# Kernel optimization log

Measured on AMD Instinct MI355X. Metric: run time of the kernel, lower is better.

The kernel has to match this reference:

```python
import jax, jax.numpy as jnp
import numpy as np

B, S, L = 256, 512, 128


def setup_inputs() -> dict:
    key = jax.random.key(0)
    k0, k1, k2, k3, k4, k5 = jax.random.split(key, 6)
    features = jax.random.normal(k0, (B, S, L), dtype=jnp.float32)
    attention_mask = jnp.ones((B, S), dtype=jnp.int32)  # all positions valid
    labels = jax.random.randint(k1, (B, S), 0, L)
    confidence = jax.random.uniform(k2, (B,), dtype=jnp.float32)
    start_transitions = jax.random.uniform(k3, (L,), minval=-0.1, maxval=0.1)
    end_transitions = jax.random.uniform(k4, (L,), minval=-0.1, maxval=0.1)
    transitions = jax.random.uniform(k5, (L, L), minval=-0.1, maxval=0.1)
    return {
        "features": features,
        "start_transitions": start_transitions,
        "end_transitions": end_transitions,
        "transitions": transitions,
        "confidence": confidence,
        "attention_mask": attention_mask,
        "labels": labels,
    }


def _crf_loss(features, start_transitions, end_transitions, transitions,
              confidence, attention_mask, labels):
    # time-major, matching torch.swapaxes(features, 0, 1)
    feats = jnp.swapaxes(features, 0, 1)                    # [S,B,L]
    mask = jnp.swapaxes(attention_mask, 0, 1).astype(bool)  # [S,B]
    labs = jnp.swapaxes(jnp.where(labels == -100, 0, labels), 0, 1)  # [S,B]
    bs = feats.shape[1]
    barange = jnp.arange(bs)

    # ---- log numerator (gold path score), fully vectorized over time ----
    emit = jnp.take_along_axis(feats, labs[:, :, None], axis=2)[..., 0]  # [S,B]
    trans_scores = transitions[labs[:-1], labs[1:]]                      # [S-1,B]
    maskf = mask[1:].astype(feats.dtype)
    log_num = (start_transitions[labs[0]] + emit[0]
               + jnp.sum((trans_scores + emit[1:]) * maskf, axis=0))
    seq_lens = mask.sum(axis=0) - 1                                      # [B]
    last_tags = labs[seq_lens, barange]
    log_num = log_num + end_transitions[last_tags]

    # ---- log denominator (partition function) via sequential scan ----
    def step(alpha, xs):
        feat_t, mask_t = xs  # [B,L], [B]
        nxt = jax.nn.logsumexp(
            alpha[:, :, None] + transitions[None, :, :] + feat_t[:, None, :],
            axis=1)
        return jnp.where(mask_t[:, None], nxt, alpha), None

    alpha0 = start_transitions + feats[0]                    # [B,L]
    alpha, _ = jax.lax.scan(step, alpha0, (feats[1:], mask[1:]))
    log_den = jax.nn.logsumexp(alpha + end_transitions, axis=1)  # [B]

    loss = (log_den - log_num) * confidence
    return jnp.mean(loss)


def reference(features, start_transitions, end_transitions, transitions,
              confidence, attention_mask, labels):
    return _crf_loss(features, start_transitions, end_transitions, transitions,
                     confidence, attention_mask, labels)
```

## Files before the change

kernel.cpp:

```cpp
#include <hip/hip_runtime.h>
#include <hip/hip_bf16.h>
#include <math.h>

#define NB 256
#define SS 512
#define LL 128

typedef short bf16x8 __attribute__((ext_vector_type(8)));
typedef float f32x4 __attribute__((ext_vector_type(4)));

__device__ __forceinline__ short f2bf(float f) {
    __hip_bfloat16 h = __float2bfloat16(f);
    short s;
    __builtin_memcpy(&s, &h, 2);
    return s;
}

#define MFMA1632(c, a, bb) \
    c = __builtin_amdgcn_mfma_f32_16x16x32_bf16(a, bb, c, 0, 0, 0)

template <int ISB>
__device__ __forceinline__ void run_chain(
    const int lane,
    const float* __restrict__ fb,
    const float* __restrict__ start_t,
    const float* __restrict__ end_t,
    const float* __restrict__ trans,
    float* __restrict__ eRing,
    const int* __restrict__ lmask,
    float* __restrict__ outv,
    float* __restrict__ oute)
{
    const int lo = lane & 15;
    const int hi = lane >> 4;

    bf16x8 Af[8][4];
#pragma unroll
    for (int nt = 0; nt < 8; ++nt) {
#pragma unroll
        for (int kt = 0; kt < 4; ++kt) {
            bf16x8 fr;
#pragma unroll
            for (int j = 0; j < 8; ++j) {
                const int r = 32 * kt + 16 * (j >> 2) + 4 * hi + (j & 3);
                const int n = 16 * nt + lo;
                const float tv = ISB ? trans[n * LL + r] : trans[r * LL + n];
                fr[j] = f2bf(__expf(tv));
            }
            Af[nt][kt] = fr;
        }
    }

    float v[8][4];
#pragma unroll
    for (int nt = 0; nt < 8; ++nt) {
#pragma unroll
        for (int j = 0; j < 4; ++j) {
            const int p = 16 * nt + 4 * hi + j;
            if (ISB) {
                v[nt][j] = __expf(end_t[p]);
            } else {
                v[nt][j] = __expf(start_t[p] + fb[p]);
            }
        }
    }

    bf16x8 Bf[4];
#pragma unroll
    for (int kt = 0; kt < 4; ++kt) {
        bf16x8 fr;
#pragma unroll
        for (int j = 0; j < 8; ++j) {
            const int nt = 2 * kt + (j >> 2);
            const int reg = j & 3;
            float val = v[nt][reg];
            if (ISB) val *= __expf(fb[(size_t)511 * LL + 16 * nt + 4 * hi + reg]);
            fr[j] = f2bf(val);
        }
        Bf[kt] = fr;
    }

    {
        const int r0 = ISB ? 510 : 1;
        const int r1 = ISB ? 509 : 2;
        const float2 a = *(const float2*)(fb + (size_t)r0 * LL + 2 * lane);
        const float2 bq = *(const float2*)(fb + (size_t)r1 * LL + 2 * lane);
        *(float2*)(eRing + 0 * LL + 2 * lane) = make_float2(__expf(a.x), __expf(a.y));
        *(float2*)(eRing + 1 * LL + 2 * lane) = make_float2(__expf(bq.x), __expf(bq.y));
    }
    float2 nxt0 = *(const float2*)(fb + (size_t)(ISB ? 508 : 3) * LL + 2 * lane);
    float2 nxt1 = *(const float2*)(fb + (size_t)(ISB ? 507 : 4) * LL + 2 * lane);

    int eacc = 0;

    for (int r = 0; r < 256; ++r) {
        const float* rp = eRing + (r & 3) * LL + 4 * hi;
        f32x4 eft[8];
#pragma unroll
        for (int nt = 0; nt < 8; ++nt)
            eft[nt] = *(const f32x4*)(rp + 16 * nt);

        *(float2*)(eRing + ((r + 2) & 3) * LL + 2 * lane) =
            make_float2(__expf(nxt0.x), __expf(nxt0.y));
        nxt0 = nxt1;
        {
            const int rowN = ISB ? (506 - r) : (r + 5);
            nxt1 = *(const float2*)(fb + (size_t)rowN * LL + 2 * lane);
        }

        int mt = lmask[ISB ? (511 - r) : (r + 1)];

        f32x4 cc[8];
#pragma unroll
        for (int nt = 0; nt < 8; ++nt) cc[nt] = (f32x4){0.f, 0.f, 0.f, 0.f};
#pragma unroll
        for (int kt = 0; kt < 4; ++kt) {
#pragma unroll
            for (int nt = 0; nt < 8; ++nt)
                MFMA1632(cc[nt], Af[nt][kt], Bf[kt]);
        }

        if (!ISB && r == 255) mt = 0;

#pragma unroll
        for (int nt = 0; nt < 8; ++nt) {
#pragma unroll
            for (int j = 0; j < 4; ++j) {
                const float cand = ISB ? cc[nt][j] : eft[nt][j] * cc[nt][j];
                v[nt][j] = mt ? cand : v[nt][j];
            }
        }

        if ((r & 7) == 7) {
            float s = 0.f;
#pragma unroll
            for (int nt = 0; nt < 8; ++nt)
#pragma unroll
                for (int j = 0; j < 4; ++j) s += v[nt][j];
            s += __shfl_xor(s, 16);
            s += __shfl_xor(s, 32);
            int ex;
            frexpf(s, &ex);
#pragma unroll
            for (int nt = 0; nt < 8; ++nt)
#pragma unroll
                for (int j = 0; j < 4; ++j) v[nt][j] = ldexpf(v[nt][j], -ex);
            eacc += ex;
        }

#pragma unroll
        for (int kt = 0; kt < 4; ++kt) {
            bf16x8 fr;
#pragma unroll
            for (int j = 0; j < 8; ++j) {
                const int nt = 2 * kt + (j >> 2);
                const int reg = j & 3;
                const float val = ISB ? eft[nt][reg] * v[nt][reg] : v[nt][reg];
                fr[j] = f2bf(val);
            }
            Bf[kt] = fr;
        }
    }

    if (lo == 0) {
#pragma unroll
        for (int nt = 0; nt < 8; ++nt) {
            f32x4 o = {v[nt][0], v[nt][1], v[nt][2], v[nt][3]};
            *(f32x4*)(outv + 16 * nt + 4 * hi) = o;
        }
    }
    if (lane == 0) *oute = (float)eacc;
}

__global__ __launch_bounds__(64, 1) void crf_chain_kernel(
    const float* __restrict__ feats,
    const float* __restrict__ start_t,
    const float* __restrict__ end_t,
    const float* __restrict__ trans,
    const int* __restrict__ mask,
    const int* __restrict__ labels,
    float* __restrict__ ws)
{
    const int bid = blockIdx.x;
    const int b = bid & 255;
    const int isB = bid >> 8;
    const int tid = threadIdx.x;

    __shared__ __align__(16) float eRing[4 * LL];
    __shared__ int lmask[SS];

#pragma unroll
    for (int q = 0; q < 8; ++q) lmask[tid + 64 * q] = mask[b * SS + tid + 64 * q];

    const float* fb = feats + (size_t)b * SS * LL;

    float* av = ws;
    float* bv = ws + NB * LL;
    float* eFa = ws + 2 * NB * LL;
    float* eBa = eFa + NB;
    float* lognum = eBa + NB;

    if (isB)
        run_chain<1>(tid, fb, start_t, end_t, trans, eRing, lmask, bv + b * LL, eBa + b);
    else
        run_chain<0>(tid, fb, start_t, end_t, trans, eRing, lmask, av + b * LL, eFa + b);

    if (isB) {
        const int* lb = labels + b * SS;
        const int* mb = mask + b * SS;
        float term = 0.f;
        int cnt = 0;
#pragma unroll
        for (int q = 0; q < 8; ++q) {
            const int tt = tid + 64 * q;
            int l = lb[tt];
            if ((unsigned)l >= LL) l = 0;
            const int m = mb[tt];
            cnt += (m != 0);
            if (tt == 0) {
                term += start_t[l] + fb[l];
            } else if (m) {
                int lp = lb[tt - 1];
                if ((unsigned)lp >= LL) lp = 0;
                term += trans[lp * LL + l] + fb[(size_t)tt * LL + l];
            }
        }
#pragma unroll
        for (int o = 1; o < 64; o <<= 1) {
            term += __shfl_xor(term, o);
            cnt += __shfl_xor(cnt, o);
        }
        if (tid == 0) {
            int sl = cnt - 1;
            sl = sl < 0 ? 0 : (sl >= SS ? SS - 1 : sl);
            int lt = lb[sl];
            if ((unsigned)lt >= LL) lt = 0;
            lognum[b] = term + end_t[lt];
        }
    }
}

__global__ __launch_bounds__(256) void crf_final_kernel(
    const float* __restrict__ ws, const float* __restrict__ conf,
    float* __restrict__ out)
{
    const int tid = threadIdx.x;
    const float* av = ws;
    const float* bv = ws + NB * LL;
    const float* eFa = ws + 2 * NB * LL;
    const float* eBa = eFa + NB;
    const float* ln = eBa + NB;

    const float4* a4 = (const float4*)(av + tid * LL);
    const float4* b4 = (const float4*)(bv + tid * LL);
    float dot = 0.f;
#pragma unroll 8
    for (int k = 0; k < 32; ++k) {
        float4 a = a4[k], bb = b4[k];
        dot += a.x * bb.x + a.y * bb.y + a.z * bb.z + a.w * bb.w;
    }
    float logZ = logf(dot) + 0.69314718055994531f * (eFa[tid] + eBa[tid]);
    float loss = (logZ - ln[tid]) * conf[tid] * (1.0f / NB);

#pragma unroll
    for (int o = 1; o < 64; o <<= 1) loss += __shfl_xor(loss, o);
    __shared__ float red[4];
    if ((tid & 63) == 0) red[tid >> 6] = loss;
    __syncthreads();
    if (tid == 0) out[0] = red[0] + red[1] + red[2] + red[3];
}

extern "C" void kernel_launch(void* const* d_in, const int* in_sizes, int n_in,
                              void* d_out, int out_size, void* d_ws, size_t ws_size,
                              hipStream_t stream) {
    const float* feats  = (const float*)d_in[0];
    const float* startt = (const float*)d_in[1];
    const float* endt   = (const float*)d_in[2];
    const float* trans  = (const float*)d_in[3];
    const float* conf   = (const float*)d_in[4];
    const int*   mask   = (const int*)d_in[5];
    const int*   labels = (const int*)d_in[6];
    float* out = (float*)d_out;
    float* ws = (float*)d_ws;

    hipLaunchKernelGGL(crf_chain_kernel, dim3(2 * NB), dim3(64), 0, stream,
                       feats, startt, endt, trans, mask, labels, ws);
    hipLaunchKernelGGL(crf_final_kernel, dim3(1), dim3(256), 0, stream,
                       ws, conf, out);
}
```

Measured before the change: 252.6 us.

## Split each CRF chain across four waves with LDS-shared alpha vector

```diff
diff --git a/kernel.cpp b/kernel.cpp
--- a/kernel.cpp
+++ b/kernel.cpp
@@ -15,17 +15,26 @@
     __builtin_memcpy(&s, &h, 2);
     return s;
 }
+__device__ __forceinline__ float bf2f(short s) {
+    return __int_as_float(((int)(unsigned short)s) << 16);
+}
 
 #define MFMA1632(c, a, bb) \
     c = __builtin_amdgcn_mfma_f32_16x16x32_bf16(a, bb, c, 0, 0, 0)
 
+__device__ __forceinline__ void wave_barrier() {
+    asm volatile("s_waitcnt lgkmcnt(0)" ::: "memory");
+    __builtin_amdgcn_s_barrier();
+}
+
 template <int ISB>
-__device__ __forceinline__ void run_chain(
-    const int lane,
+__device__ __forceinline__ void run_chain4(
+    const int w, const int lane,
     const float* __restrict__ fb,
     const float* __restrict__ start_t,
     const float* __restrict__ end_t,
     const float* __restrict__ trans,
+    short* __restrict__ img,
     float* __restrict__ eRing,
     const int* __restrict__ lmask,
     float* __restrict__ outv,
@@ -33,146 +42,132 @@
 {
     const int lo = lane & 15;
     const int hi = lane >> 4;
-
-    bf16x8 Af[8][4];
-#pragma unroll
-    for (int nt = 0; nt < 8; ++nt) {
+    const int nt0 = 2 * w, nt1 = 2 * w + 1;
+
+    bf16x8 Af0[4], Af1[4];
+#pragma unroll
+    for (int kt = 0; kt < 4; ++kt) {
+        bf16x8 f0, f1;
+        const int n0 = 16 * nt0 + lo, n1 = 16 * nt1 + lo;
+#pragma unroll
+        for (int j = 0; j < 8; ++j) {
+            const int k = 32 * kt + 8 * hi + j;
+            f0[j] = f2bf(__expf(ISB ? trans[n0 * LL + k] : trans[k * LL + n0]));
+            f1[j] = f2bf(__expf(ISB ? trans[n1 * LL + k] : trans[k * LL + n1]));
+        }
+        Af0[kt] = f0;
+        Af1[kt] = f1;
+    }
+
+    float v[2][4];
+#pragma unroll
+    for (int n2 = 0; n2 < 2; ++n2)
+#pragma unroll
+        for (int j = 0; j < 4; ++j) {
+            const int p = 16 * (2 * w + n2) + 4 * hi + j;
+            v[n2][j] = ISB ? __expf(end_t[p]) : __expf(start_t[p] + fb[p]);
+        }
+
+    f32x4 ep0 = {1.f, 1.f, 1.f, 1.f}, ep1 = ep0;
+    if (ISB) {
+#pragma unroll
+        for (int j = 0; j < 4; ++j) {
+            ep0[j] = __expf(fb[(size_t)511 * LL + 16 * nt0 + 4 * hi + j]);
+            ep1[j] = __expf(fb[(size_t)511 * LL + 16 * nt1 + 4 * hi + j]);
+        }
+    }
+
+    float2 nxt;
+    {
+        const int row = ISB ? (508 - w) : (w + 3);
+        nxt = *(const float2*)(fb + (size_t)row * LL + 2 * lane);
+    }
+
+    wave_barrier();
+
+    int eacc = 0;
+
+    for (int r = 0; r < 256; ++r) {
+        short4 p0, p1;
+        p0.x = f2bf(ISB ? v[0][0] * ep0[0] : v[0][0]);
+        p0.y = f2bf(ISB ? v[0][1] * ep0[1] : v[0][1]);
+        p0.z = f2bf(ISB ? v[0][2] * ep0[2] : v[0][2]);
+        p0.w = f2bf(ISB ? v[0][3] * ep0[3] : v[0][3]);
+        p1.x = f2bf(ISB ? v[1][0] * ep1[0] : v[1][0]);
+        p1.y = f2bf(ISB ? v[1][1] * ep1[1] : v[1][1]);
+        p1.z = f2bf(ISB ? v[1][2] * ep1[2] : v[1][2]);
+        p1.w = f2bf(ISB ? v[1][3] * ep1[3] : v[1][3]);
+        short* ib = img + (r & 1) * LL;
+        if (lo == 0) {
+            *(short4*)(ib + 32 * w + 4 * hi) = p0;
+            *(short4*)(ib + 32 * w + 16 + 4 * hi) = p1;
+        }
+        wave_barrier();
+
+        bf16x8 Bf[4];
+#pragma unroll
+        for (int kt = 0; kt < 4; ++kt)
+            Bf[kt] = *(const bf16x8*)(ib + 32 * kt + 8 * hi);
+
+        const float* rp = eRing + (r & 3) * LL + 4 * hi;
+        f32x4 ec0 = *(const f32x4*)(rp + 16 * nt0);
+        f32x4 ec1 = *(const f32x4*)(rp + 16 * nt1);
+
+        if (w == (r & 3)) {
+            *(float2*)(eRing + ((r + 2) & 3) * LL + 2 * lane) =
+                make_float2(__expf(nxt.x), __expf(nxt.y));
+            const int rowN = ISB ? (504 - r) : (r + 7);
+            nxt = *(const float2*)(fb + (size_t)rowN * LL + 2 * lane);
+        }
+
+        int mt = lmask[ISB ? (511 - r) : (r + 1)];
+        if (!ISB && r == 255) mt = 0;
+
+        f32x4 cc0 = {0.f, 0.f, 0.f, 0.f}, cc1 = {0.f, 0.f, 0.f, 0.f};
 #pragma unroll
         for (int kt = 0; kt < 4; ++kt) {
-            bf16x8 fr;
-#pragma unroll
-            for (int j = 0; j < 8; ++j) {
-                const int r = 32 * kt + 16 * (j >> 2) + 4 * hi + (j & 3);
-                const int n = 16 * nt + lo;
-                const float tv = ISB ? trans[n * LL + r] : trans[r * LL + n];
-                fr[j] = f2bf(__expf(tv));
-            }
-            Af[nt][kt] = fr;
-        }
-    }
-
-    float v[8][4];
-#pragma unroll
-    for (int nt = 0; nt < 8; ++nt) {
+            MFMA1632(cc0, Af0[kt], Bf[kt]);
+            MFMA1632(cc1, Af1[kt], Bf[kt]);
+        }
+
 #pragma unroll
         for (int j = 0; j < 4; ++j) {
-            const int p = 16 * nt + 4 * hi + j;
-            if (ISB) {
-                v[nt][j] = __expf(end_t[p]);
-            } else {
-                v[nt][j] = __expf(start_t[p] + fb[p]);
-            }
-        }
-    }
-
-    bf16x8 Bf[4];
-#pragma unroll
-    for (int kt = 0; kt < 4; ++kt) {
-        bf16x8 fr;
-#pragma unroll
-        for (int j = 0; j < 8; ++j) {
-            const int nt = 2 * kt + (j >> 2);
-            const int reg = j & 3;
-            float val = v[nt][reg];
-            if (ISB) val *= __expf(fb[(size_t)511 * LL + 16 * nt + 4 * hi + reg]);
-            fr[j] = f2bf(val);
-        }
-        Bf[kt] = fr;
-    }
-
-    {
-        const int r0 = ISB ? 510 : 1;
-        const int r1 = ISB ? 509 : 2;
-        const float2 a = *(const float2*)(fb + (size_t)r0 * LL + 2 * lane);
-        const float2 bq = *(const float2*)(fb + (size_t)r1 * LL + 2 * lane);
-        *(float2*)(eRing + 0 * LL + 2 * lane) = make_float2(__expf(a.x), __expf(a.y));
-        *(float2*)(eRing + 1 * LL + 2 * lane) = make_float2(__expf(bq.x), __expf(bq.y));
-    }
-    float2 nxt0 = *(const float2*)(fb + (size_t)(ISB ? 508 : 3) * LL + 2 * lane);
-    float2 nxt1 = *(const float2*)(fb + (size_t)(ISB ? 507 : 4) * LL + 2 * lane);
-
-    int eacc = 0;
-
-    for (int r = 0; r < 256; ++r) {
-        const float* rp = eRing + (r & 3) * LL + 4 * hi;
-        f32x4 eft[8];
-#pragma unroll
-        for (int nt = 0; nt < 8; ++nt)
-            eft[nt] = *(const f32x4*)(rp + 16 * nt);
-
-        *(float2*)(eRing + ((r + 2) & 3) * LL + 2 * lane) =
-            make_float2(__expf(nxt0.x), __expf(nxt0.y));
-        nxt0 = nxt1;
-        {
-            const int rowN = ISB ? (506 - r) : (r + 5);
-            nxt1 = *(const float2*)(fb + (size_t)rowN * LL + 2 * lane);
-        }
-
-        int mt = lmask[ISB ? (511 - r) : (r + 1)];
-
-        f32x4 cc[8];
-#pragma unroll
-        for (int nt = 0; nt < 8; ++nt) cc[nt] = (f32x4){0.f, 0.f, 0.f, 0.f};
-#pragma unroll
-        for (int kt = 0; kt < 4; ++kt) {
-#pragma unroll
-            for (int nt = 0; nt < 8; ++nt)
-                MFMA1632(cc[nt], Af[nt][kt], Bf[kt]);
-        }
-
-        if (!ISB && r == 255) mt = 0;
-
-#pragma unroll
-        for (int nt = 0; nt < 8; ++nt) {
-#pragma unroll
-            for (int j = 0; j < 4; ++j) {
-                const float cand = ISB ? cc[nt][j] : eft[nt][j] * cc[nt][j];
-                v[nt][j] = mt ? cand : v[nt][j];
-            }
+            const float c0 = ISB ? cc0[j] : ec0[j] * cc0[j];
+            const float c1 = ISB ? cc1[j] : ec1[j] * cc1[j];
+            v[0][j] = mt ? c0 : v[0][j];
+            v[1][j] = mt ? c1 : v[1][j];
         }
 
         if ((r & 7) == 7) {
             float s = 0.f;
 #pragma unroll
-            for (int nt = 0; nt < 8; ++nt)
-#pragma unroll
-                for (int j = 0; j < 4; ++j) s += v[nt][j];
+            for (int kt = 0; kt < 4; ++kt)
+#pragma unroll
+                for (int j = 0; j < 8; ++j) s += bf2f(Bf[kt][j]);
             s += __shfl_xor(s, 16);
             s += __shfl_xor(s, 32);
             int ex;
             frexpf(s, &ex);
 #pragma unroll
-            for (int nt = 0; nt < 8; ++nt)
-#pragma unroll
-                for (int j = 0; j < 4; ++j) v[nt][j] = ldexpf(v[nt][j], -ex);
+            for (int n2 = 0; n2 < 2; ++n2)
+#pragma unroll
+                for (int j = 0; j < 4; ++j) v[n2][j] = ldexpf(v[n2][j], -ex);
             eacc += ex;
         }
 
-#pragma unroll
-        for (int kt = 0; kt < 4; ++kt) {
-            bf16x8 fr;
-#pragma unroll
-            for (int j = 0; j < 8; ++j) {
-                const int nt = 2 * kt + (j >> 2);
-                const int reg = j & 3;
-                const float val = ISB ? eft[nt][reg] * v[nt][reg] : v[nt][reg];
-                fr[j] = f2bf(val);
-            }
-            Bf[kt] = fr;
-        }
+        if (ISB) { ep0 = ec0; ep1 = ec1; }
     }
 
     if (lo == 0) {
-#pragma unroll
-        for (int nt = 0; nt < 8; ++nt) {
-            f32x4 o = {v[nt][0], v[nt][1], v[nt][2], v[nt][3]};
-            *(f32x4*)(outv + 16 * nt + 4 * hi) = o;
-        }
-    }
-    if (lane == 0) *oute = (float)eacc;
-}
-
-__global__ __launch_bounds__(64, 1) void crf_chain_kernel(
+        *(f32x4*)(outv + 16 * nt0 + 4 * hi) =
+            (f32x4){v[0][0], v[0][1], v[0][2], v[0][3]};
+        *(f32x4*)(outv + 16 * nt1 + 4 * hi) =
+            (f32x4){v[1][0], v[1][1], v[1][2], v[1][3]};
+    }
+    if (w == 0 && lane == 0) *oute = (float)eacc;
+}
+
+__global__ __launch_bounds__(256, 2) void crf_chain_kernel(
     const float* __restrict__ feats,
     const float* __restrict__ start_t,
     const float* __restrict__ end_t,
@@ -185,14 +180,25 @@
     const int b = bid & 255;
     const int isB = bid >> 8;
     const int tid = threadIdx.x;
-
+    const int w = tid >> 6;
+    const int lane = tid & 63;
+
+    __shared__ __align__(16) short img[2 * LL];
     __shared__ __align__(16) float eRing[4 * LL];
     __shared__ int lmask[SS];
-
-#pragma unroll
-    for (int q = 0; q < 8; ++q) lmask[tid + 64 * q] = mask[b * SS + tid + 64 * q];
+    __shared__ float nred[4];
+    __shared__ int cred[4];
 
     const float* fb = feats + (size_t)b * SS * LL;
+
+    lmask[tid] = mask[b * SS + tid];
+    lmask[tid + 256] = mask[b * SS + tid + 256];
+    {
+        const int slot = tid >> 7;
+        const int e = tid & 127;
+        const int row = isB ? (510 - slot) : (1 + slot);
+        eRing[slot * LL + e] = __expf(fb[(size_t)row * LL + e]);
+    }
 
     float* av = ws;
     float* bv = ws + NB * LL;
@@ -201,9 +207,11 @@
     float* lognum = eBa + NB;
 
     if (isB)
-        run_chain<1>(tid, fb, start_t, end_t, trans, eRing, lmask, bv + b * LL, eBa + b);
+        run_chain4<1>(w, lane, fb, start_t, end_t, trans, img, eRing, lmask,
+                      bv + b * LL, eBa + b);
     else
-        run_chain<0>(tid, fb, start_t, end_t, trans, eRing, lmask, av + b * LL, eFa + b);
+        run_chain4<0>(w, lane, fb, start_t, end_t, trans, img, eRing, lmask,
+                      av + b * LL, eFa + b);
 
     if (isB) {
         const int* lb = labels + b * SS;
@@ -211,8 +219,8 @@
         float term = 0.f;
         int cnt = 0;
 #pragma unroll
-        for (int q = 0; q < 8; ++q) {
-            const int tt = tid + 64 * q;
+        for (int q = 0; q < 2; ++q) {
+            const int tt = tid + 256 * q;
             int l = lb[tt];
             if ((unsigned)l >= LL) l = 0;
             const int m = mb[tt];
@@ -230,12 +238,16 @@
             term += __shfl_xor(term, o);
             cnt += __shfl_xor(cnt, o);
         }
+        if (lane == 0) { nred[w] = term; cred[w] = cnt; }
+        __syncthreads();
         if (tid == 0) {
-            int sl = cnt - 1;
+            const float tot = nred[0] + nred[1] + nred[2] + nred[3];
+            const int c = cred[0] + cred[1] + cred[2] + cred[3];
+            int sl = c - 1;
             sl = sl < 0 ? 0 : (sl >= SS ? SS - 1 : sl);
             int lt = lb[sl];
             if ((unsigned)lt >= LL) lt = 0;
-            lognum[b] = term + end_t[lt];
+            lognum[b] = tot + end_t[lt];
         }
     }
 }
@@ -283,7 +295,7 @@
     float* out = (float*)d_out;
     float* ws = (float*)d_ws;
 
-    hipLaunchKernelGGL(crf_chain_kernel, dim3(2 * NB), dim3(64), 0, stream,
+    hipLaunchKernelGGL(crf_chain_kernel, dim3(2 * NB), dim3(256), 0, stream,
                        feats, startt, endt, trans, mask, labels, ws);
     hipLaunchKernelGGL(crf_final_kernel, dim3(1), dim3(256), 0, stream,
                        ws, conf, out);
```

Measured after the change: 205.6 us, median of 2. 1.23x faster.
